# Kernel optimization log

Hardware: AMD Instinct MI355X
Metric: run time of the kernel (lower is better)

Reference implementation:

```python
import jax, jax.numpy as jnp
import numpy as np

WORLD_SIZE = 1
EXPERT_NUM = 8
D_MODEL = 1024
D_HIDDEN = 4096
TOK_PER_EXPERT = 2048


def setup_inputs() -> dict:
    key = jax.random.key(0)
    k1, k2, k3 = jax.random.split(key, 3)
    x = jax.random.normal(k1, (EXPERT_NUM, TOK_PER_EXPERT, D_MODEL), dtype=jnp.float32)
    # kaiming_uniform-like scale for faithfulness of magnitudes
    bound1 = 1.0 / np.sqrt(D_MODEL)
    bound2 = 1.0 / np.sqrt(D_HIDDEN)
    weight1 = jax.random.uniform(k2, (EXPERT_NUM, D_HIDDEN, D_MODEL), dtype=jnp.float32, minval=-bound1, maxval=bound1)
    weight2 = jax.random.uniform(k3, (EXPERT_NUM, D_MODEL, D_HIDDEN), dtype=jnp.float32, minval=-bound2, maxval=bound2)
    return {"x": x, "weight1": weight1, "weight2": weight2}


def reference(x, weight1, weight2):
    # x -> (world_size, expert_num, tokens, d_model)
    xr = x.reshape(WORLD_SIZE, EXPERT_NUM, -1, D_MODEL)
    # grouped GEMM 1 + ReLU: [g,e,s,m] x [e,h,m] -> [g,e,s,h]
    ffn1 = jax.nn.relu(jnp.einsum('gesm,ehm->gesh', xr, weight1))
    # grouped GEMM 2: [g,e,s,h] x [e,m,h] -> [g,e,s,m]
    y = jnp.einsum('gesh,emh->gesm', ffn1, weight2)
    return y
```

## Files before the change

kernel.cpp:

```cpp
#include <hip/hip_runtime.h>
#include <hip/hip_bf16.h>

#define EXPERTS 8
#define TOK 2048
#define DM 1024
#define DH 4096

#define BM 128
#define BN 128
#define BK 32
#define LSTR 40

typedef __bf16 bf16x8 __attribute__((ext_vector_type(8)));
typedef float  f32x4  __attribute__((ext_vector_type(4)));

static __device__ __forceinline__ bf16x8 cvt8(float4 a, float4 b) {
    bf16x8 r;
    r[0] = (__bf16)a.x; r[1] = (__bf16)a.y; r[2] = (__bf16)a.z; r[3] = (__bf16)a.w;
    r[4] = (__bf16)b.x; r[5] = (__bf16)b.y; r[6] = (__bf16)b.z; r[7] = (__bf16)b.w;
    return r;
}

static __device__ __forceinline__ void gload16(const __bf16* g, __bf16* l) {
    __builtin_amdgcn_global_load_lds(
        (__attribute__((address_space(1))) void*)g,
        (__attribute__((address_space(3))) void*)l, 16, 0, 0);
}

#define BARRIER() asm volatile("s_barrier" ::: "memory")
#define LGKM0()   do { asm volatile("s_waitcnt lgkmcnt(0)" ::: "memory"); \
                       __builtin_amdgcn_sched_barrier(0); } while (0)
#define VMW8()    asm volatile("s_waitcnt vmcnt(8)" ::: "memory")
#define VMW0()    asm volatile("s_waitcnt vmcnt(0)" ::: "memory")

__global__ __launch_bounds__(256)
void cvt_bf16(const float* __restrict__ in, __bf16* __restrict__ out, int n8) {
    int i = blockIdx.x * blockDim.x + threadIdx.x;
    const int stride = gridDim.x * blockDim.x;
    for (; i < n8; i += stride) {
        const float4* p = (const float4*)in + (size_t)i * 2;
        float4 a = p[0], b = p[1];
        *((bf16x8*)out + i) = cvt8(a, b);
    }
}

template<bool RELU, bool OUT_BF16>
__global__ __launch_bounds__(512, 2)
void gemm8(const __bf16* __restrict__ Ap, const __bf16* __restrict__ Bp,
           void* __restrict__ Cp, int N, int K, int tiles_m, int tiles_n,
           size_t sA, size_t sB, size_t sC)
{
    __shared__ __bf16 lds[2][2][16384];

    int bid = blockIdx.x;
    const int chunk = gridDim.x >> 3;
    bid = (bid & 7) * chunk + (bid >> 3);

    const int per_e = tiles_m * tiles_n;
    const int e  = bid / per_e;
    const int tt = bid - e * per_e;
    const int tn = tt / tiles_m;
    const int tm = tt - tn * tiles_m;

    const int tid = threadIdx.x;
    const int l   = tid & 63;
    const int wid = tid >> 6;
    const int wr  = wid >> 2;
    const int wc  = wid & 3;
    const int lr  = l & 15;
    const int kg  = l >> 4;
    const int lq  = l >> 3;
    const int swz_e = ((l & 7) ^ lq) << 3;

    const int cc0  = (kg * 16) ^ ((l & 7) << 4);
    const int cc1  = cc0 ^ 64;
    const int rowA = (wr * 128 + lr) * 128;
    const int rowB = (wc * 64  + lr) * 128;

    const __bf16* Ag = Ap + e * sA + (size_t)(tm * 256) * K;
    const __bf16* Bg = Bp + e * sB + (size_t)(tn * 256) * K;

    auto stage_half = [&](const __bf16* g, int mat, int c2, int h, int kt2) {
        const __bf16* s0 = g + (size_t)(h * 128 + wid * 8 + lq) * K + kt2 * 64 + swz_e;
        gload16(s0,                   &lds[c2][mat][h * 8192 + wid * 512]);
        gload16(s0 + (size_t)64 * K,  &lds[c2][mat][h * 8192 + 4096 + wid * 512]);
    };

    f32x4 acc[8][4];
    #pragma unroll
    for (int m = 0; m < 8; ++m)
        #pragma unroll
        for (int n = 0; n < 4; ++n)
            acc[m][n] = (f32x4){0.f, 0.f, 0.f, 0.f};

    const int NT = K / 64;

    stage_half(Ag, 0, 0, 0, 0); stage_half(Ag, 0, 0, 1, 0);
    stage_half(Bg, 1, 0, 0, 0); stage_half(Bg, 1, 0, 1, 0);
    stage_half(Ag, 0, 1, 0, 1); stage_half(Ag, 0, 1, 1, 1);
    stage_half(Bg, 1, 1, 0, 1); stage_half(Bg, 1, 1, 1, 1);
    VMW8();
    BARRIER();

    for (int t = 0; t < NT; ++t) {
        const int c = t & 1;
        const char* Ab = (const char*)&lds[c][0][0] + rowA;
        const char* Bb = (const char*)&lds[c][1][0] + rowB;
        const bool pf = (t + 2 < NT);

        bf16x8 a[4][2], b0[2][2], b1[2][2];

        #pragma unroll
        for (int mf = 0; mf < 4; ++mf) {
            a[mf][0] = *(const bf16x8*)(Ab + mf * 2048 + cc0);
            a[mf][1] = *(const bf16x8*)(Ab + mf * 2048 + cc1);
        }
        #pragma unroll
        for (int nf = 0; nf < 2; ++nf) {
            b0[nf][0] = *(const bf16x8*)(Bb + nf * 2048 + cc0);
            b0[nf][1] = *(const bf16x8*)(Bb + nf * 2048 + cc1);
        }
        BARRIER();
        __builtin_amdgcn_s_setprio(1);
        #pragma unroll
        for (int mf = 0; mf < 4; ++mf)
            #pragma unroll
            for (int nf = 0; nf < 2; ++nf) {
                acc[mf][nf] = __builtin_amdgcn_mfma_f32_16x16x32_bf16(a[mf][0], b0[nf][0], acc[mf][nf], 0, 0, 0);
                acc[mf][nf] = __builtin_amdgcn_mfma_f32_16x16x32_bf16(a[mf][1], b0[nf][1], acc[mf][nf], 0, 0, 0);
            }
        __builtin_amdgcn_s_setprio(0);
        LGKM0();
        BARRIER();

        #pragma unroll
        for (int nf = 0; nf < 2; ++nf) {
            b1[nf][0] = *(const bf16x8*)(Bb + (2 + nf) * 2048 + cc0);
            b1[nf][1] = *(const bf16x8*)(Bb + (2 + nf) * 2048 + cc1);
        }
        BARRIER();
        __builtin_amdgcn_s_setprio(1);
        #pragma unroll
        for (int mf = 0; mf < 4; ++mf)
            #pragma unroll
            for (int nf = 0; nf < 2; ++nf) {
                acc[mf][2 + nf] = __builtin_amdgcn_mfma_f32_16x16x32_bf16(a[mf][0], b1[nf][0], acc[mf][2 + nf], 0, 0, 0);
                acc[mf][2 + nf] = __builtin_amdgcn_mfma_f32_16x16x32_bf16(a[mf][1], b1[nf][1], acc[mf][2 + nf], 0, 0, 0);
            }
        __builtin_amdgcn_s_setprio(0);
        LGKM0();
        BARRIER();

        #pragma unroll
        for (int mf = 0; mf < 4; ++mf) {
            a[mf][0] = *(const bf16x8*)(Ab + (4 + mf) * 2048 + cc0);
            a[mf][1] = *(const bf16x8*)(Ab + (4 + mf) * 2048 + cc1);
        }
        if (pf) { stage_half(Bg, 1, c, 0, t + 2); stage_half(Bg, 1, c, 1, t + 2); }
        BARRIER();
        __builtin_amdgcn_s_setprio(1);
        #pragma unroll
        for (int mf = 0; mf < 4; ++mf)
            #pragma unroll
            for (int nf = 0; nf < 2; ++nf) {
                acc[4 + mf][2 + nf] = __builtin_amdgcn_mfma_f32_16x16x32_bf16(a[mf][0], b1[nf][0], acc[4 + mf][2 + nf], 0, 0, 0);
                acc[4 + mf][2 + nf] = __builtin_amdgcn_mfma_f32_16x16x32_bf16(a[mf][1], b1[nf][1], acc[4 + mf][2 + nf], 0, 0, 0);
            }
        __builtin_amdgcn_s_setprio(0);
        LGKM0();
        BARRIER();

        if (pf) { stage_half(Ag, 0, c, 0, t + 2); stage_half(Ag, 0, c, 1, t + 2); }
        BARRIER();
        __builtin_amdgcn_s_setprio(1);
        #pragma unroll
        for (int mf = 0; mf < 4; ++mf)
            #pragma unroll
            for (int nf = 0; nf < 2; ++nf) {
                acc[4 + mf][nf] = __builtin_amdgcn_mfma_f32_16x16x32_bf16(a[mf][0], b0[nf][0], acc[4 + mf][nf], 0, 0, 0);
                acc[4 + mf][nf] = __builtin_amdgcn_mfma_f32_16x16x32_bf16(a[mf][1], b0[nf][1], acc[4 + mf][nf], 0, 0, 0);
            }
        __builtin_amdgcn_s_setprio(0);
        LGKM0();
        if (t + 1 < NT) { if (pf) VMW8(); else VMW0(); }
        BARRIER();
    }

    const int orow = tm * 256 + wr * 128 + kg * 4;
    const int ocol = tn * 256 + wc * 64 + lr;
    if constexpr (OUT_BF16) {
        __bf16* C = (__bf16*)Cp + e * sC;
        #pragma unroll
        for (int mf = 0; mf < 8; ++mf)
            #pragma unroll
            for (int j = 0; j < 4; ++j) {
                const size_t base = (size_t)(orow + mf * 16 + j) * N + ocol;
                #pragma unroll
                for (int nf = 0; nf < 4; ++nf) {
                    float v = acc[mf][nf][j];
                    if (RELU) v = fmaxf(v, 0.f);
                    C[base + nf * 16] = (__bf16)v;
                }
            }
    } else {
        float* C = (float*)Cp + e * sC;
        #pragma unroll
        for (int mf = 0; mf < 8; ++mf)
            #pragma unroll
            for (int j = 0; j < 4; ++j) {
                const size_t base = (size_t)(orow + mf * 16 + j) * N + ocol;
                #pragma unroll
                for (int nf = 0; nf < 4; ++nf) {
                    float v = acc[mf][nf][j];
                    if (RELU) v = fmaxf(v, 0.f);
                    C[base + nf * 16] = v;
                }
            }
    }
}

template<int AMODE, int BMODE, bool RELU, bool OUT_BF16>
__global__ __launch_bounds__(256)
void gemm2(const void* __restrict__ Ap, const void* __restrict__ Bp,
           void* __restrict__ Cp, int N, int K, int tiles_m, int tiles_n,
           size_t sA, size_t sB, size_t sC)
{
    constexpr int LA = (AMODE == 0) ? BK : LSTR;
    constexpr int LB = (BMODE == 0) ? BK : LSTR;
    __shared__ __bf16 As[BM * LA];
    __shared__ __bf16 Bs[BN * LB];

    int bid = blockIdx.x;
    const int chunk = gridDim.x >> 3;
    bid = (bid & 7) * chunk + (bid >> 3);

    const int per_e = tiles_m * tiles_n;
    const int e  = bid / per_e;
    const int t  = bid - e * per_e;
    const int tn = t / tiles_m;
    const int tm = t - tn * tiles_m;

    const int tid = threadIdx.x;
    const int l   = tid & 63;
    const int wid = tid >> 6;
    const int wr  = wid >> 1, wc = wid & 1;
    const int lr  = l & 15;
    const int kg  = l >> 4;
    const int srow = tid >> 1;
    const int scol = (tid & 1) << 4;

    const __bf16* gA = nullptr; __bf16* lA = nullptr;
    const float*  pAf = nullptr; __bf16* aWr = nullptr;
    float4 A0, A1, A2, A3;
    if constexpr (AMODE == 0) {
        gA = (const __bf16*)Ap + e * sA
           + (size_t)(tm * BM + wid * 16 + (l >> 2)) * K + (l & 3) * 8;
        lA = As + wid * 512;
    } else {
        pAf = (const float*)Ap + e * sA + (size_t)(tm * BM + srow) * K + scol;
        aWr = As + srow * LA + scol;
        A0 = *(const float4*)(pAf);      A1 = *(const float4*)(pAf + 4);
        A2 = *(const float4*)(pAf + 8);  A3 = *(const float4*)(pAf + 12);
    }
    const __bf16* gB = nullptr; __bf16* lB = nullptr;
    const float*  pBf = nullptr; __bf16* bWr = nullptr;
    float4 B0, B1, B2, B3;
    if constexpr (BMODE == 0) {
        gB = (const __bf16*)Bp + e * sB
           + (size_t)(tn * BN + wid * 16 + (l >> 2)) * K + (l & 3) * 8;
        lB = Bs + wid * 512;
    } else {
        pBf = (const float*)Bp + e * sB + (size_t)(tn * BN + srow) * K + scol;
        bWr = Bs + srow * LB + scol;
        B0 = *(const float4*)(pBf);      B1 = *(const float4*)(pBf + 4);
        B2 = *(const float4*)(pBf + 8);  B3 = *(const float4*)(pBf + 12);
    }

    const __bf16* aRd = As + (wr * 64 + lr) * LA + kg * 8;
    const __bf16* bRd = Bs + (wc * 64 + lr) * LB + kg * 8;

    f32x4 acc[4][4];
    #pragma unroll
    for (int m = 0; m < 4; ++m)
        #pragma unroll
        for (int n = 0; n < 4; ++n)
            acc[m][n] = (f32x4){0.f, 0.f, 0.f, 0.f};

    const int NT = K / BK;
    for (int kt = 0; kt < NT; ++kt) {
        if (kt) __syncthreads();
        if constexpr (AMODE == 0) {
            gload16(gA, lA);
            gload16(gA + (size_t)64 * K, lA + 2048);
            gA += BK;
        } else {
            *(bf16x8*)(aWr)     = cvt8(A0, A1);
            *(bf16x8*)(aWr + 8) = cvt8(A2, A3);
        }
        if constexpr (BMODE == 0) {
            gload16(gB, lB);
            gload16(gB + (size_t)64 * K, lB + 2048);
            gB += BK;
        } else {
            *(bf16x8*)(bWr)     = cvt8(B0, B1);
            *(bf16x8*)(bWr + 8) = cvt8(B2, B3);
        }
        __syncthreads();

        if (kt + 1 < NT) {
            if constexpr (AMODE == 2) {
                pAf += BK;
                A0 = *(const float4*)(pAf);      A1 = *(const float4*)(pAf + 4);
                A2 = *(const float4*)(pAf + 8);  A3 = *(const float4*)(pAf + 12);
            }
            if constexpr (BMODE == 2) {
                pBf += BK;
                B0 = *(const float4*)(pBf);      B1 = *(const float4*)(pBf + 4);
                B2 = *(const float4*)(pBf + 8);  B3 = *(const float4*)(pBf + 12);
            }
        }

        bf16x8 af[4], bfr[4];
        #pragma unroll
        for (int m = 0; m < 4; ++m) af[m]  = *(const bf16x8*)(aRd + m * 16 * LA);
        #pragma unroll
        for (int n = 0; n < 4; ++n) bfr[n] = *(const bf16x8*)(bRd + n * 16 * LB);
        #pragma unroll
        for (int m = 0; m < 4; ++m)
            #pragma unroll
            for (int n = 0; n < 4; ++n)
                acc[m][n] = __builtin_amdgcn_mfma_f32_16x16x32_bf16(af[m], bfr[n], acc[m][n], 0, 0, 0);
    }

    const int orow = tm * BM + wr * 64 + kg * 4;
    const int ocol = tn * BN + wc * 64 + lr;
    if constexpr (OUT_BF16) {
        __bf16* C = (__bf16*)Cp + e * sC;
        #pragma unroll
        for (int m = 0; m < 4; ++m)
            #pragma unroll
            for (int j = 0; j < 4; ++j) {
                const size_t base = (size_t)(orow + m * 16 + j) * N + ocol;
                #pragma unroll
                for (int n = 0; n < 4; ++n) {
                    float v = acc[m][n][j];
                    if (RELU) v = fmaxf(v, 0.f);
                    C[base + n * 16] = (__bf16)v;
                }
            }
    } else {
        float* C = (float*)Cp + e * sC;
        #pragma unroll
        for (int m = 0; m < 4; ++m)
            #pragma unroll
            for (int j = 0; j < 4; ++j) {
                const size_t base = (size_t)(orow + m * 16 + j) * N + ocol;
                #pragma unroll
                for (int n = 0; n < 4; ++n) {
                    float v = acc[m][n][j];
                    if (RELU) v = fmaxf(v, 0.f);
                    C[base + n * 16] = v;
                }
            }
    }
}

extern "C" void kernel_launch(void* const* d_in, const int* in_sizes, int n_in,
                              void* d_out, int out_size, void* d_ws, size_t ws_size,
                              hipStream_t stream) {
    const float* x  = (const float*)d_in[0];
    const float* w1 = (const float*)d_in[1];
    const float* w2 = (const float*)d_in[2];
    float* out = (float*)d_out;

    const size_t SZ_F  = (size_t)EXPERTS * TOK * DH * sizeof(__bf16);
    const size_t SZ_X  = (size_t)EXPERTS * TOK * DM * sizeof(__bf16);
    const size_t SZ_W1 = (size_t)EXPERTS * DH * DM * sizeof(__bf16);
    const size_t SZ_W2 = (size_t)EXPERTS * DM * DH * sizeof(__bf16);

    char* wsb = (char*)d_ws;
    __bf16* ffn1 = (__bf16*)wsb;

    const dim3 blk(256);
    const dim3 cgrid(2048);
    const int NX  = EXPERTS * TOK * DM / 8;
    const int NW1 = EXPERTS * DH * DM / 8;
    const int NW2 = EXPERTS * DM * DH / 8;

    const size_t eA1 = (size_t)TOK * DM, eB1 = (size_t)DH * DM, eC1 = (size_t)TOK * DH;
    const size_t eA2 = (size_t)TOK * DH, eB2 = (size_t)DM * DH, eC2 = (size_t)TOK * DM;

    if (ws_size >= SZ_F + SZ_X + SZ_W1 + SZ_W2) {
        __bf16* xb  = (__bf16*)(wsb + SZ_F);
        __bf16* w1b = (__bf16*)(wsb + SZ_F + SZ_X);
        __bf16* w2b = (__bf16*)(wsb + SZ_F + SZ_X + SZ_W1);
        hipLaunchKernelGGL(cvt_bf16, cgrid, blk, 0, stream, x, xb, NX);
        hipLaunchKernelGGL(cvt_bf16, cgrid, blk, 0, stream, w1, w1b, NW1);
        hipLaunchKernelGGL(cvt_bf16, cgrid, blk, 0, stream, w2, w2b, NW2);
        const dim3 g1(EXPERTS * (TOK / 256) * (DH / 256));
        const dim3 g2(EXPERTS * (TOK / 256) * (DM / 256));
        hipLaunchKernelGGL((gemm8<true, true>), g1, dim3(512), 0, stream,
            xb, w1b, ffn1, DH, DM, TOK / 256, DH / 256, eA1, eB1, eC1);
        hipLaunchKernelGGL((gemm8<false, false>), g2, dim3(512), 0, stream,
            ffn1, w2b, out, DM, DH, TOK / 256, DM / 256, eA2, eB2, eC2);
    } else if (ws_size >= SZ_F + SZ_X + SZ_W1) {
        __bf16* xb  = (__bf16*)(wsb + SZ_F);
        __bf16* w1b = (__bf16*)(wsb + SZ_F + SZ_X);
        hipLaunchKernelGGL(cvt_bf16, cgrid, blk, 0, stream, x, xb, NX);
        hipLaunchKernelGGL(cvt_bf16, cgrid, blk, 0, stream, w1, w1b, NW1);
        const dim3 g1(EXPERTS * (TOK / BM) * (DH / BN));
        const dim3 g2(EXPERTS * (TOK / BM) * (DM / BN));
        hipLaunchKernelGGL((gemm2<0, 0, true, true>), g1, blk, 0, stream,
            xb, w1b, ffn1, DH, DM, TOK / BM, DH / BN, eA1, eB1, eC1);
        hipLaunchKernelGGL((gemm2<0, 2, false, false>), g2, blk, 0, stream,
            ffn1, w2, out, DM, DH, TOK / BM, DM / BN, eA2, eB2, eC2);
    } else if (ws_size >= SZ_F + SZ_W1) {
        __bf16* w1b = (__bf16*)(wsb + SZ_F);
        hipLaunchKernelGGL(cvt_bf16, cgrid, blk, 0, stream, w1, w1b, NW1);
        const dim3 g1(EXPERTS * (TOK / BM) * (DH / BN));
        const dim3 g2(EXPERTS * (TOK / BM) * (DM / BN));
        hipLaunchKernelGGL((gemm2<2, 0, true, true>), g1, blk, 0, stream,
            x, w1b, ffn1, DH, DM, TOK / BM, DH / BN, eA1, eB1, eC1);
        hipLaunchKernelGGL((gemm2<0, 2, false, false>), g2, blk, 0, stream,
            ffn1, w2, out, DM, DH, TOK / BM, DM / BN, eA2, eB2, eC2);
    } else if (ws_size >= SZ_F) {
        const dim3 g1(EXPERTS * (TOK / BM) * (DH / BN));
        const dim3 g2(EXPERTS * (TOK / BM) * (DM / BN));
        hipLaunchKernelGGL((gemm2<2, 2, true, true>), g1, blk, 0, stream,
            x, w1, ffn1, DH, DM, TOK / BM, DH / BN, eA1, eB1, eC1);
        hipLaunchKernelGGL((gemm2<0, 2, false, false>), g2, blk, 0, stream,
            ffn1, w2, out, DM, DH, TOK / BM, DM / BN, eA2, eB2, eC2);
    } else {
        int rows = (int)((ws_size / ((size_t)DH * sizeof(__bf16))) / BM) * BM;
        if (rows <= 0) rows = BM;
        if (rows > TOK) rows = TOK;
        for (int e = 0; e < EXPERTS; ++e) {
            for (int r0 = 0; r0 < TOK; r0 += rows) {
                int mr = (TOK - r0 < rows) ? (TOK - r0) : rows;
                dim3 cg1((mr / BM) * (DH / BN));
                hipLaunchKernelGGL((gemm2<2, 2, true, true>), cg1, blk, 0, stream,
                    x + ((size_t)e * TOK + r0) * DM, w1 + (size_t)e * DH * DM, ffn1,
                    DH, DM, mr / BM, DH / BN, (size_t)0, (size_t)0, (size_t)0);
                dim3 cg2((mr / BM) * (DM / BN));
                hipLaunchKernelGGL((gemm2<0, 2, false, false>), cg2, blk, 0, stream,
                    ffn1, w2 + (size_t)e * DM * DH, out + ((size_t)e * TOK + r0) * DM,
                    DM, DH, mr / BM, DM / BN, (size_t)0, (size_t)0, (size_t)0);
            }
        }
    }
}
```

Before: 382.3 us.

## Software-pipeline LDS fragment loads across MFMA phases and fuse conversion kernels

Restructures the gemm8 main loop so LDS fragment reads for the next phase, and for the next K-tile's first A/B fragments, are issued before the current MFMA block runs. It waits with partial lgkmcnt counts instead of full drains, which removes several barriers per iteration and lets LDS latency overlap with MFMA work. The three fp32-to-bf16 conversion launches are merged into one kernel, saving launch overhead and tail effects. It also routes a fallback path to gemm8. The risks are higher register pressure from the extra a2 fragment buffer, and subtle ordering hazards between prefetch writes into the buffer being consumed.

```diff
diff --git a/kernel.cpp b/kernel.cpp
--- a/kernel.cpp
+++ b/kernel.cpp
@@ -28,19 +28,26 @@
 }
 
 #define BARRIER() asm volatile("s_barrier" ::: "memory")
-#define LGKM0()   do { asm volatile("s_waitcnt lgkmcnt(0)" ::: "memory"); \
+#define LGKMC(n)  do { asm volatile("s_waitcnt lgkmcnt(" #n ")" ::: "memory"); \
                        __builtin_amdgcn_sched_barrier(0); } while (0)
 #define VMW8()    asm volatile("s_waitcnt vmcnt(8)" ::: "memory")
 #define VMW0()    asm volatile("s_waitcnt vmcnt(0)" ::: "memory")
 
 __global__ __launch_bounds__(256)
-void cvt_bf16(const float* __restrict__ in, __bf16* __restrict__ out, int n8) {
+void cvt_all(const float* __restrict__ x,  const float* __restrict__ w1,
+             const float* __restrict__ w2, __bf16* __restrict__ xb,
+             __bf16* __restrict__ w1b,     __bf16* __restrict__ w2b,
+             int nx, int nw1, int ntot) {
     int i = blockIdx.x * blockDim.x + threadIdx.x;
     const int stride = gridDim.x * blockDim.x;
-    for (; i < n8; i += stride) {
-        const float4* p = (const float4*)in + (size_t)i * 2;
+    for (; i < ntot; i += stride) {
+        const float* src; __bf16* dst; int off;
+        if (i < nx)            { src = x;  dst = xb;  off = i; }
+        else if (i < nx + nw1) { src = w1; dst = w1b; off = i - nx; }
+        else                   { src = w2; dst = w2b; off = i - nx - nw1; }
+        const float4* p = (const float4*)src + (size_t)off * 2;
         float4 a = p[0], b = p[1];
-        *((bf16x8*)out + i) = cvt8(a, b);
+        *((bf16x8*)dst + off) = cvt8(a, b);
     }
 }
 
@@ -82,8 +89,8 @@
 
     auto stage_half = [&](const __bf16* g, int mat, int c2, int h, int kt2) {
         const __bf16* s0 = g + (size_t)(h * 128 + wid * 8 + lq) * K + kt2 * 64 + swz_e;
-        gload16(s0,                   &lds[c2][mat][h * 8192 + wid * 512]);
-        gload16(s0 + (size_t)64 * K,  &lds[c2][mat][h * 8192 + 4096 + wid * 512]);
+        gload16(s0,                  &lds[c2][mat][h * 8192 + wid * 512]);
+        gload16(s0 + (size_t)64 * K, &lds[c2][mat][h * 8192 + 4096 + wid * 512]);
     };
 
     f32x4 acc[8][4];
@@ -102,14 +109,10 @@
     VMW8();
     BARRIER();
 
-    for (int t = 0; t < NT; ++t) {
-        const int c = t & 1;
-        const char* Ab = (const char*)&lds[c][0][0] + rowA;
-        const char* Bb = (const char*)&lds[c][1][0] + rowB;
-        const bool pf = (t + 2 < NT);
-
-        bf16x8 a[4][2], b0[2][2], b1[2][2];
-
+    bf16x8 a[4][2], a2[4][2], b0[2][2], b1[2][2];
+    {
+        const char* Ab = (const char*)&lds[0][0][0] + rowA;
+        const char* Bb = (const char*)&lds[0][1][0] + rowB;
         #pragma unroll
         for (int mf = 0; mf < 4; ++mf) {
             a[mf][0] = *(const bf16x8*)(Ab + mf * 2048 + cc0);
@@ -120,6 +123,23 @@
             b0[nf][0] = *(const bf16x8*)(Bb + nf * 2048 + cc0);
             b0[nf][1] = *(const bf16x8*)(Bb + nf * 2048 + cc1);
         }
+    }
+
+    for (int t = 0; t < NT; ++t) {
+        const int c = t & 1;
+        const char* Ab  = (const char*)&lds[c][0][0] + rowA;
+        const char* Bb  = (const char*)&lds[c][1][0] + rowB;
+        const char* Abn = (const char*)&lds[c ^ 1][0][0] + rowA;
+        const char* Bbn = (const char*)&lds[c ^ 1][1][0] + rowB;
+        const bool pf   = (t + 2 < NT);
+        const bool more = (t + 1 < NT);
+
+        #pragma unroll
+        for (int nf = 0; nf < 2; ++nf) {
+            b1[nf][0] = *(const bf16x8*)(Bb + (2 + nf) * 2048 + cc0);
+            b1[nf][1] = *(const bf16x8*)(Bb + (2 + nf) * 2048 + cc1);
+        }
+        LGKMC(4);
         BARRIER();
         __builtin_amdgcn_s_setprio(1);
         #pragma unroll
@@ -130,15 +150,15 @@
                 acc[mf][nf] = __builtin_amdgcn_mfma_f32_16x16x32_bf16(a[mf][1], b0[nf][1], acc[mf][nf], 0, 0, 0);
             }
         __builtin_amdgcn_s_setprio(0);
-        LGKM0();
+
+        #pragma unroll
+        for (int mf = 0; mf < 4; ++mf) {
+            a2[mf][0] = *(const bf16x8*)(Ab + (4 + mf) * 2048 + cc0);
+            a2[mf][1] = *(const bf16x8*)(Ab + (4 + mf) * 2048 + cc1);
+        }
+        LGKMC(8);
         BARRIER();
-
-        #pragma unroll
-        for (int nf = 0; nf < 2; ++nf) {
-            b1[nf][0] = *(const bf16x8*)(Bb + (2 + nf) * 2048 + cc0);
-            b1[nf][1] = *(const bf16x8*)(Bb + (2 + nf) * 2048 + cc1);
-        }
-        BARRIER();
+        if (pf) { stage_half(Bg, 1, c, 0, t + 2); stage_half(Bg, 1, c, 1, t + 2); }
         __builtin_amdgcn_s_setprio(1);
         #pragma unroll
         for (int mf = 0; mf < 4; ++mf)
@@ -148,42 +168,45 @@
                 acc[mf][2 + nf] = __builtin_amdgcn_mfma_f32_16x16x32_bf16(a[mf][1], b1[nf][1], acc[mf][2 + nf], 0, 0, 0);
             }
         __builtin_amdgcn_s_setprio(0);
-        LGKM0();
+
+        LGKMC(0);
         BARRIER();
-
-        #pragma unroll
-        for (int mf = 0; mf < 4; ++mf) {
-            a[mf][0] = *(const bf16x8*)(Ab + (4 + mf) * 2048 + cc0);
-            a[mf][1] = *(const bf16x8*)(Ab + (4 + mf) * 2048 + cc1);
-        }
-        if (pf) { stage_half(Bg, 1, c, 0, t + 2); stage_half(Bg, 1, c, 1, t + 2); }
+        if (pf) { stage_half(Ag, 0, c, 0, t + 2); stage_half(Ag, 0, c, 1, t + 2); }
+        __builtin_amdgcn_s_setprio(1);
+        #pragma unroll
+        for (int mf = 0; mf < 4; ++mf)
+            #pragma unroll
+            for (int nf = 0; nf < 2; ++nf) {
+                acc[4 + mf][2 + nf] = __builtin_amdgcn_mfma_f32_16x16x32_bf16(a2[mf][0], b1[nf][0], acc[4 + mf][2 + nf], 0, 0, 0);
+                acc[4 + mf][2 + nf] = __builtin_amdgcn_mfma_f32_16x16x32_bf16(a2[mf][1], b1[nf][1], acc[4 + mf][2 + nf], 0, 0, 0);
+            }
+        __builtin_amdgcn_s_setprio(0);
+
+        if (more) { if (pf) VMW8(); else VMW0(); }
         BARRIER();
+        if (more) {
+            #pragma unroll
+            for (int mf = 0; mf < 4; ++mf) {
+                a[mf][0] = *(const bf16x8*)(Abn + mf * 2048 + cc0);
+                a[mf][1] = *(const bf16x8*)(Abn + mf * 2048 + cc1);
+            }
+        }
         __builtin_amdgcn_s_setprio(1);
         #pragma unroll
         for (int mf = 0; mf < 4; ++mf)
             #pragma unroll
             for (int nf = 0; nf < 2; ++nf) {
-                acc[4 + mf][2 + nf] = __builtin_amdgcn_mfma_f32_16x16x32_bf16(a[mf][0], b1[nf][0], acc[4 + mf][2 + nf], 0, 0, 0);
-                acc[4 + mf][2 + nf] = __builtin_amdgcn_mfma_f32_16x16x32_bf16(a[mf][1], b1[nf][1], acc[4 + mf][2 + nf], 0, 0, 0);
+                acc[4 + mf][nf] = __builtin_amdgcn_mfma_f32_16x16x32_bf16(a2[mf][0], b0[nf][0], acc[4 + mf][nf], 0, 0, 0);
+                acc[4 + mf][nf] = __builtin_amdgcn_mfma_f32_16x16x32_bf16(a2[mf][1], b0[nf][1], acc[4 + mf][nf], 0, 0, 0);
             }
         __builtin_amdgcn_s_setprio(0);
-        LGKM0();
-        BARRIER();
-
-        if (pf) { stage_half(Ag, 0, c, 0, t + 2); stage_half(Ag, 0, c, 1, t + 2); }
-        BARRIER();
-        __builtin_amdgcn_s_setprio(1);
-        #pragma unroll
-        for (int mf = 0; mf < 4; ++mf)
+        if (more) {
             #pragma unroll
             for (int nf = 0; nf < 2; ++nf) {
-                acc[4 + mf][nf] = __builtin_amdgcn_mfma_f32_16x16x32_bf16(a[mf][0], b0[nf][0], acc[4 + mf][nf], 0, 0, 0);
-                acc[4 + mf][nf] = __builtin_amdgcn_mfma_f32_16x16x32_bf16(a[mf][1], b0[nf][1], acc[4 + mf][nf], 0, 0, 0);
-            }
-        __builtin_amdgcn_s_setprio(0);
-        LGKM0();
-        if (t + 1 < NT) { if (pf) VMW8(); else VMW0(); }
-        BARRIER();
+                b0[nf][0] = *(const bf16x8*)(Bbn + nf * 2048 + cc0);
+                b0[nf][1] = *(const bf16x8*)(Bbn + nf * 2048 + cc1);
+            }
+        }
     }
 
     const int orow = tm * 256 + wr * 128 + kg * 4;
@@ -394,9 +417,8 @@
         __bf16* xb  = (__bf16*)(wsb + SZ_F);
         __bf16* w1b = (__bf16*)(wsb + SZ_F + SZ_X);
         __bf16* w2b = (__bf16*)(wsb + SZ_F + SZ_X + SZ_W1);
-        hipLaunchKernelGGL(cvt_bf16, cgrid, blk, 0, stream, x, xb, NX);
-        hipLaunchKernelGGL(cvt_bf16, cgrid, blk, 0, stream, w1, w1b, NW1);
-        hipLaunchKernelGGL(cvt_bf16, cgrid, blk, 0, stream, w2, w2b, NW2);
+        hipLaunchKernelGGL(cvt_all, cgrid, blk, 0, stream,
+            x, w1, w2, xb, w1b, w2b, NX, NW1, NX + NW1 + NW2);
         const dim3 g1(EXPERTS * (TOK / 256) * (DH / 256));
         const dim3 g2(EXPERTS * (TOK / 256) * (DM / 256));
         hipLaunchKernelGGL((gemm8<true, true>), g1, dim3(512), 0, stream,
@@ -406,17 +428,18 @@
     } else if (ws_size >= SZ_F + SZ_X + SZ_W1) {
         __bf16* xb  = (__bf16*)(wsb + SZ_F);
         __bf16* w1b = (__bf16*)(wsb + SZ_F + SZ_X);
-        hipLaunchKernelGGL(cvt_bf16, cgrid, blk, 0, stream, x, xb, NX);
-        hipLaunchKernelGGL(cvt_bf16, cgrid, blk, 0, stream, w1, w1b, NW1);
-        const dim3 g1(EXPERTS * (TOK / BM) * (DH / BN));
+        hipLaunchKernelGGL(cvt_all, cgrid, blk, 0, stream,
+            x, w1, w1, xb, w1b, w1b, NX, NW1, NX + NW1);
+        const dim3 g1(EXPERTS * (TOK / 256) * (DH / 256));
         const dim3 g2(EXPERTS * (TOK / BM) * (DM / BN));
-        hipLaunchKernelGGL((gemm2<0, 0, true, true>), g1, blk, 0, stream,
-            xb, w1b, ffn1, DH, DM, TOK / BM, DH / BN, eA1, eB1, eC1);
+        hipLaunchKernelGGL((gemm8<true, true>), g1, dim3(512), 0, stream,
+            xb, w1b, ffn1, DH, DM, TOK / 256, DH / 256, eA1, eB1, eC1);
         hipLaunchKernelGGL((gemm2<0, 2, false, false>), g2, blk, 0, stream,
             ffn1, w2, out, DM, DH, TOK / BM, DM / BN, eA2, eB2, eC2);
     } else if (ws_size >= SZ_F + SZ_W1) {
         __bf16* w1b = (__bf16*)(wsb + SZ_F);
-        hipLaunchKernelGGL(cvt_bf16, cgrid, blk, 0, stream, w1, w1b, NW1);
+        hipLaunchKernelGGL(cvt_all, cgrid, blk, 0, stream,
+            w1, w1, w1, w1b, w1b, w1b, NW1, 0, NW1);
         const dim3 g1(EXPERTS * (TOK / BM) * (DH / BN));
         const dim3 g2(EXPERTS * (TOK / BM) * (DM / BN));
         hipLaunchKernelGGL((gemm2<2, 0, true, true>), g1, blk, 0, stream,
```

Result: faster. 364.5 us (-4.7%).
